# Performance work log

Measured on AMD Instinct MI355X. Metric: run time of the kernel, lower is better.

The kernel has to match this reference:

```python
import jax, jax.numpy as jnp
import numpy as np

EPS = 1e-5
B, C, H, W = 128, 512, 32, 32


def setup_inputs() -> dict:
    key = jax.random.key(0)
    ks = jax.random.split(key, 3)
    s = 1.0 / np.sqrt(C)
    return {
        "x": jax.random.normal(ks[0], (B, C, H, W), dtype=jnp.float32),
        "ln_w": jnp.ones((C, H, W), dtype=jnp.float32),
        "ln_b": jnp.zeros((C, H, W), dtype=jnp.float32),
        "w1": jax.random.uniform(ks[1], (C, C), dtype=jnp.float32, minval=-s, maxval=s),
        "b1": jnp.zeros((C,), dtype=jnp.float32),
        "w2": jax.random.uniform(ks[2], (C, C), dtype=jnp.float32, minval=-s, maxval=s),
        "b2": jnp.zeros((C,), dtype=jnp.float32),
    }


def reference(x, ln_w, ln_b, w1, b1, w2, b2):
    b, c, h, w = x.shape
    # LayerNorm over the full (C, H, W) feature volume per sample
    mu = jnp.mean(x, axis=(1, 2, 3), keepdims=True)
    var = jnp.mean(jnp.square(x - mu), axis=(1, 2, 3), keepdims=True)
    xn = (x - mu) * jax.lax.rsqrt(var + EPS) * ln_w + ln_b
    # tokens: (B, H*W, C)
    t = xn.reshape(b, c, h * w).transpose(0, 2, 1)
    hdn = jax.nn.relu(jnp.einsum('bsc,dc->bsd', t, w1) + b1)
    out = jnp.einsum('bsd,ed->bse', hdn, w2) + b2
    return out.transpose(0, 2, 1).reshape(b, c, h, w)
```

## Files before the change

### kernel.cpp

```cpp
#include <hip/hip_runtime.h>
#include <stdint.h>


#define NSAMP 128
#define CCH   512
#define HWSZ  1024
#define NPER  (CCH*HWSZ)

typedef unsigned short u16;
typedef __bf16 bf16x8 __attribute__((ext_vector_type(8)));
typedef float  f32x4  __attribute__((ext_vector_type(4)));

__device__ __forceinline__ float b2f(u16 h){ return __uint_as_float(((unsigned)h)<<16); }
__device__ __forceinline__ u16 f2b(float f){
  unsigned u = __float_as_uint(f);
  u += 0x7FFFu + ((u>>16)&1u);
  return (u16)(u>>16);
}
__device__ __forceinline__ void unpack8(uint4 v, float* f){
  const unsigned* u = (const unsigned*)&v;
#pragma unroll
  for (int q=0;q<4;q++){
    f[2*q]   = __uint_as_float(u[q]<<16);
    f[2*q+1] = __uint_as_float(u[q]&0xFFFF0000u);
  }
}
__device__ __forceinline__ void load8(const void* base, size_t idx, int isf, float* f){
  if (isf){
    const float* p = (const float*)base + idx;
    uint4 a = *(const uint4*)p;
    uint4 b = *(const uint4*)(p+4);
    const float* af = (const float*)&a;
    const float* bf = (const float*)&b;
#pragma unroll
    for (int j=0;j<4;j++){ f[j]=af[j]; f[4+j]=bf[j]; }
  } else {
    uint4 v = *(const uint4*)((const u16*)base + idx);
    unpack8(v, f);
  }
}
__device__ __forceinline__ void store8b(u16* dst, const float* f){
  uint4 o; unsigned* ou = (unsigned*)&o;
#pragma unroll
  for (int q=0;q<4;q++) ou[q] = (unsigned)f2b(f[2*q]) | ((unsigned)f2b(f[2*q+1])<<16);
  *(uint4*)dst = o;
}

__device__ __forceinline__ void gload_lds16(const u16* g, u16* l){
  __builtin_amdgcn_global_load_lds(
      (const __attribute__((address_space(1))) void*)g,
      (__attribute__((address_space(3))) void*)l,
      16, 0, 0);
}

__global__ __launch_bounds__(256) void detect_kernel(const u16* __restrict__ x,
                                                     int* __restrict__ flag){
  __shared__ int sh[256];
  int tid = threadIdx.x, cnt = 0;
  for (int i=tid; i<16384; i+=256){
    unsigned e = ((unsigned)x[i] >> 7) & 0xFFu;
    cnt += (e >= 0xC0u);
  }
  sh[tid] = cnt; __syncthreads();
  for (int s=128; s; s>>=1){ if (tid<s) sh[tid]+=sh[tid+s]; __syncthreads(); }
  if (tid==0) flag[0] = sh[0];
}

__global__ __launch_bounds__(256) void convert_kernel(
    const void* __restrict__ w1, const void* __restrict__ w2,
    const void* __restrict__ b1, const void* __restrict__ b2,
    const int* __restrict__ flag,
    u16* __restrict__ w1b, u16* __restrict__ w2b,
    float* __restrict__ b1f, float* __restrict__ b2f){
  int isf = flag[0] > 64;
  int t = blockIdx.x*256 + threadIdx.x;
  size_t i8 = (size_t)t*8;
  float f[8];
  load8(w1, i8, isf, f); store8b(w1b + i8, f);
  load8(w2, i8, isf, f); store8b(w2b + i8, f);
  if (t < 64){
    load8(b1, i8, isf, f);
#pragma unroll
    for (int j=0;j<8;j++) b1f[i8+j] = f[j];
    load8(b2, i8, isf, f);
#pragma unroll
    for (int j=0;j<8;j++) b2f[i8+j] = f[j];
  }
}

__global__ __launch_bounds__(256) void stats_kernel(const void* __restrict__ x,
                                                    float* __restrict__ stats,
                                                    const int* __restrict__ flag){
  int isf = flag[0] > 64;
  int b   = blockIdx.y;
  int blk = blockIdx.x;
  size_t base = (size_t)b*NPER + (size_t)blk*32768;
  int tid = threadIdx.x;
  float s1 = 0.f, s2 = 0.f;
#pragma unroll
  for (int i=0;i<16;i++){
    float f[8];
    load8(x, base + i*2048 + tid*8, isf, f);
#pragma unroll
    for (int j=0;j<8;j++){ s1 += f[j]; s2 += f[j]*f[j]; }
  }
#pragma unroll
  for (int off=32; off; off>>=1){
    s1 += __shfl_down(s1, off);
    s2 += __shfl_down(s2, off);
  }
  __shared__ float r1[4], r2[4];
  int w = tid>>6, lane = tid&63;
  if (lane==0){ r1[w]=s1; r2[w]=s2; }
  __syncthreads();
  if (tid==0){
    atomicAdd(&stats[2*b],   r1[0]+r1[1]+r1[2]+r1[3]);
    atomicAdd(&stats[2*b+1], r2[0]+r2[1]+r2[2]+r2[3]);
  }
}

__global__ __launch_bounds__(256) void lnT_kernel(const void* __restrict__ x,
                                                  const void* __restrict__ lw,
                                                  const void* __restrict__ lb,
                                                  const float* __restrict__ stats,
                                                  const int* __restrict__ flag,
                                                  int gb0,
                                                  u16* __restrict__ xnT){
  int isf = flag[0] > 64;
  int bl = blockIdx.z;
  int gb = gb0 + bl;
  int c0 = blockIdx.y*64;
  int s0 = blockIdx.x*64;
  const float invN = 1.f/(float)NPER;
  float mu  = stats[2*gb]*invN;
  float var = fmaxf(stats[2*gb+1]*invN - mu*mu, 0.f);
  float rs  = rsqrtf(var + 1e-5f);

  __shared__ float T[64][65];
  int tid = threadIdx.x;
  int tr  = tid>>3;
  int tcl = (tid&7)*8;

#pragma unroll
  for (int p=0;p<2;p++){
    int c = c0 + p*32 + tr;
    size_t idx = (size_t)c*HWSZ + s0 + tcl;
    float xf[8], wf[8], bf_[8];
    load8(x,  (size_t)gb*NPER + idx, isf, xf);
    load8(lw, idx, isf, wf);
    load8(lb, idx, isf, bf_);
    float* dst = &T[p*32 + tr][tcl];
#pragma unroll
    for (int j=0;j<8;j++) dst[j] = (xf[j]-mu)*rs*wf[j] + bf_[j];
  }
  __syncthreads();
#pragma unroll
  for (int p=0;p<2;p++){
    int srow = p*32 + tr;
    float tmp[8];
#pragma unroll
    for (int j=0;j<8;j++) tmp[j] = T[tcl+j][srow];
    store8b(xnT + ((size_t)bl*HWSZ + s0 + srow)*CCH + c0 + tcl, tmp);
  }
}

template<int RELU, int BIASM, int MFIRST, int NOUT, int DUALOUT>
__global__ __launch_bounds__(256) void gemm_kernel(
    const u16* __restrict__ A, long sA,
    const u16* __restrict__ B, long sB,
    const float* __restrict__ bias,
    u16* __restrict__ Co,
    const int* __restrict__ flag, int gb0)
{
  __shared__ __align__(16) u16 sh[32768];

  int b  = blockIdx.y;
  int bx = blockIdx.x;
  int tm, tn;
  if (MFIRST){ tm = bx & 7; tn = bx >> 3; }
  else       { tn = bx & 7; tm = bx >> 3; }
  const u16* Ab = A + (size_t)b*sA + (size_t)(tm*128)*512;
  const u16* Bb = B + (size_t)b*sB + (size_t)(tn*128)*512;

  int tid  = threadIdx.x;
  int lane = tid & 63;
  int w    = tid >> 6;
  int wm   = w >> 1, wn = w & 1;
  int l15  = lane & 15;
  int q    = lane >> 4;
  int sw   = l15 & 7;

  int ar  = tid >> 3;
  int acs = ((tid & 7) ^ (ar & 7)) * 8;
  const u16* aSrc = Ab + (size_t)ar*512 + acs;
  const u16* bSrc = Bb + (size_t)ar*512 + acs;

  f32x4 acc[4][4];
#pragma unroll
  for (int i=0;i<4;i++)
#pragma unroll
    for (int j=0;j<4;j++) acc[i][j] = (f32x4){0.f,0.f,0.f,0.f};

  auto STAGE = [&](int p, int kk){
    u16* aD = sh + p*16384 + tid*8;
    u16* bD = sh + p*16384 + 8192 + tid*8;
#pragma unroll
    for (int j=0;j<4;j++) gload_lds16(aSrc + j*16384 + kk, aD + j*2048);
#pragma unroll
    for (int j=0;j<4;j++) gload_lds16(bSrc + j*16384 + kk, bD + j*2048);
  };
  auto COMPUTE = [&](int p){
    const u16* Asb = sh + p*16384;
    const u16* Bsb = sh + p*16384 + 8192;
#pragma unroll
    for (int ks=0; ks<2; ks++){
      bf16x8 fa[4], fb[4];
      int pc = ((ks*4 + q) ^ sw) * 8;
#pragma unroll
      for (int i=0;i<4;i++){
        fa[i] = *(const bf16x8*)(Asb + (wm*64 + i*16 + l15)*64 + pc);
        fb[i] = *(const bf16x8*)(Bsb + (wn*64 + i*16 + l15)*64 + pc);
      }
#pragma unroll
      for (int i=0;i<4;i++)
#pragma unroll
        for (int jn=0;jn<4;jn++)
          acc[i][jn] = __builtin_amdgcn_mfma_f32_16x16x32_bf16(fa[i], fb[jn], acc[i][jn], 0,0,0);
    }
  };

  STAGE(0, 0);
  __syncthreads();
#pragma unroll
  for (int t=0; t<7; t++){
    int cur = t & 1;
    STAGE(cur ^ 1, (t+1)*64);
    COMPUTE(cur);
    __syncthreads();
  }
  COMPUTE(7 & 1);
  __syncthreads();

  int isf = DUALOUT ? (flag[0] > 64) : 0;
  size_t sampOff = (size_t)(gb0 + b) * NPER;
  int row0 = tm*128, col0 = tn*128;

  if (!DUALOUT || !isf){
    u16* Cb = Co + sampOff;
#pragma unroll
    for (int i=0;i<4;i++){
#pragma unroll
      for (int jn=0;jn<4;jn++){
        int n = wn*64 + jn*16 + l15;
        float bn = BIASM ? 0.f : bias[col0 + n];
#pragma unroll
        for (int r=0;r<4;r++){
          int m = wm*64 + i*16 + q*4 + r;
          float v = acc[i][jn][r] + (BIASM ? bias[row0 + m] : bn);
          if (RELU) v = fmaxf(v, 0.f);
          sh[m*128 + (n ^ ((m&7)<<3))] = f2b(v);
        }
      }
    }
    __syncthreads();
    int rr  = tid >> 1;
    int c0_ = (tid & 1)*8;
#pragma unroll
    for (int j=0;j<8;j++){
      int c = c0_ + j;
      uint4 vv = *(const uint4*)(sh + rr*128 + ((c ^ (rr&7))<<3));
      *(uint4*)(Cb + (size_t)(row0+rr)*NOUT + col0 + (c<<3)) = vv;
    }
  } else {
    float* Cf  = (float*)Co + sampOff;
    float* shf = (float*)sh;
#pragma unroll
    for (int p=0;p<2;p++){
      if (p) __syncthreads();
      if (wm == p){
#pragma unroll
        for (int i=0;i<4;i++){
#pragma unroll
          for (int jn=0;jn<4;jn++){
            int n = wn*64 + jn*16 + l15;
            float bn = BIASM ? 0.f : bias[col0 + n];
#pragma unroll
            for (int r=0;r<4;r++){
              int ml = i*16 + q*4 + r;
              float v = acc[i][jn][r] + (BIASM ? bias[row0 + p*64 + ml] : bn);
              if (RELU) v = fmaxf(v, 0.f);
              shf[ml*128 + (((n>>2) ^ (ml&7))<<2) + (n&3)] = v;
            }
          }
        }
      }
      __syncthreads();
      int rr = tid >> 2, qt = tid & 3;
#pragma unroll
      for (int j=0;j<8;j++){
        int c = qt*8 + j;
        uint4 vv = *(const uint4*)(shf + rr*128 + ((c ^ (rr&7))<<2));
        *(uint4*)(Cf + (size_t)(row0 + p*64 + rr)*NOUT + col0 + (c<<2)) = vv;
      }
    }
  }
}

extern "C" void kernel_launch(void* const* d_in, const int* in_sizes, int n_in,
                              void* d_out, int out_size, void* d_ws, size_t ws_size,
                              hipStream_t stream) {
  (void)in_sizes; (void)n_in; (void)out_size;
  const void* x  = d_in[0];
  const void* lw = d_in[1];
  const void* lb = d_in[2];
  const void* w1 = d_in[3];
  const void* b1 = d_in[4];
  const void* w2 = d_in[5];
  const void* b2 = d_in[6];

  char* ws = (char*)d_ws;
  float* stats = (float*)ws;
  int*   flag  = (int*)(ws + 1024);
  float* b1f   = (float*)(ws + 2048);
  float* b2f   = (float*)(ws + 4096);
  u16*   w1b   = (u16*)(ws + 8192);
  u16*   w2b   = (u16*)(ws + 8192 + 524288);
  u16*   xnT   = (u16*)(ws + (size_t)(2u<<20));

  long gmax = ((long)ws_size - (2L<<20)) / (2L<<20);
  int G = (int)(gmax < 1 ? 1 : (gmax > 128 ? 128 : gmax));
  u16* hdnT = xnT + (size_t)G*NPER;

  hipMemsetAsync(d_ws, 0, 2048, stream);
  detect_kernel<<<1,256,0,stream>>>((const u16*)x, flag);
  convert_kernel<<<128,256,0,stream>>>(w1, w2, b1, b2, flag, w1b, w2b, b1f, b2f);
  stats_kernel<<<dim3(16,NSAMP),256,0,stream>>>(x, stats, flag);

  for (int b0=0; b0<NSAMP; b0+=G){
    int Gi = (NSAMP-b0 < G) ? (NSAMP-b0) : G;
    lnT_kernel<<<dim3(HWSZ/64, CCH/64, Gi),256,0,stream>>>(x, lw, lb, stats, flag, b0, xnT);
    gemm_kernel<1,0,1,512,0><<<dim3(32,Gi),256,0,stream>>>(
        xnT, (long)NPER, w1b, 0L, b1f, hdnT, flag, 0);
    gemm_kernel<0,1,0,1024,1><<<dim3(32,Gi),256,0,stream>>>(
        w2b, 0L, hdnT, (long)NPER, b2f, (u16*)d_out, flag, b0);
  }
}
```

Measured before the change: 813.3 us.

## Pre-convert LN affine params to bf16, relax GEMM pipeline barriers, widen fp32 epilogue

```diff
diff --git a/kernel.cpp b/kernel.cpp
--- a/kernel.cpp
+++ b/kernel.cpp
@@ -69,15 +69,21 @@
 __global__ __launch_bounds__(256) void convert_kernel(
     const void* __restrict__ w1, const void* __restrict__ w2,
     const void* __restrict__ b1, const void* __restrict__ b2,
+    const void* __restrict__ lw, const void* __restrict__ lb,
     const int* __restrict__ flag,
     u16* __restrict__ w1b, u16* __restrict__ w2b,
-    float* __restrict__ b1f, float* __restrict__ b2f){
+    float* __restrict__ b1f, float* __restrict__ b2f,
+    u16* __restrict__ lwb, u16* __restrict__ lbb){
   int isf = flag[0] > 64;
   int t = blockIdx.x*256 + threadIdx.x;
   size_t i8 = (size_t)t*8;
   float f[8];
-  load8(w1, i8, isf, f); store8b(w1b + i8, f);
-  load8(w2, i8, isf, f); store8b(w2b + i8, f);
+  if (t < 32768){
+    load8(w1, i8, isf, f); store8b(w1b + i8, f);
+    load8(w2, i8, isf, f); store8b(w2b + i8, f);
+  }
+  load8(lw, i8, isf, f); store8b(lwb + i8, f);
+  load8(lb, i8, isf, f); store8b(lbb + i8, f);
   if (t < 64){
     load8(b1, i8, isf, f);
 #pragma unroll
@@ -120,8 +126,8 @@
 }
 
 __global__ __launch_bounds__(256) void lnT_kernel(const void* __restrict__ x,
-                                                  const void* __restrict__ lw,
-                                                  const void* __restrict__ lb,
+                                                  const u16* __restrict__ lwb,
+                                                  const u16* __restrict__ lbb,
                                                   const float* __restrict__ stats,
                                                   const int* __restrict__ flag,
                                                   int gb0,
@@ -146,9 +152,9 @@
     int c = c0 + p*32 + tr;
     size_t idx = (size_t)c*HWSZ + s0 + tcl;
     float xf[8], wf[8], bf_[8];
-    load8(x,  (size_t)gb*NPER + idx, isf, xf);
-    load8(lw, idx, isf, wf);
-    load8(lb, idx, isf, bf_);
+    load8(x, (size_t)gb*NPER + idx, isf, xf);
+    unpack8(*(const uint4*)(lwb + idx), wf);
+    unpack8(*(const uint4*)(lbb + idx), bf_);
     float* dst = &T[p*32 + tr][tcl];
 #pragma unroll
     for (int j=0;j<8;j++) dst[j] = (xf[j]-mu)*rs*wf[j] + bf_[j];
@@ -230,15 +236,19 @@
   };
 
   STAGE(0, 0);
-  __syncthreads();
 #pragma unroll
   for (int t=0; t<7; t++){
-    int cur = t & 1;
-    STAGE(cur ^ 1, (t+1)*64);
-    COMPUTE(cur);
-    __syncthreads();
-  }
-  COMPUTE(7 & 1);
+    STAGE((t+1)&1, (t+1)*64);
+    asm volatile("s_waitcnt vmcnt(8)" ::: "memory");
+    __builtin_amdgcn_s_barrier();
+    __builtin_amdgcn_sched_barrier(0);
+    COMPUTE(t & 1);
+    __builtin_amdgcn_s_barrier();
+  }
+  asm volatile("s_waitcnt vmcnt(0)" ::: "memory");
+  __builtin_amdgcn_s_barrier();
+  __builtin_amdgcn_sched_barrier(0);
+  COMPUTE(1);
   __syncthreads();
 
   int isf = DUALOUT ? (flag[0] > 64) : 0;
@@ -275,33 +285,28 @@
     float* Cf  = (float*)Co + sampOff;
     float* shf = (float*)sh;
 #pragma unroll
-    for (int p=0;p<2;p++){
-      if (p) __syncthreads();
-      if (wm == p){
-#pragma unroll
-        for (int i=0;i<4;i++){
-#pragma unroll
-          for (int jn=0;jn<4;jn++){
-            int n = wn*64 + jn*16 + l15;
-            float bn = BIASM ? 0.f : bias[col0 + n];
-#pragma unroll
-            for (int r=0;r<4;r++){
-              int ml = i*16 + q*4 + r;
-              float v = acc[i][jn][r] + (BIASM ? bias[row0 + p*64 + ml] : bn);
-              if (RELU) v = fmaxf(v, 0.f);
-              shf[ml*128 + (((n>>2) ^ (ml&7))<<2) + (n&3)] = v;
-            }
-          }
+    for (int i=0;i<4;i++){
+#pragma unroll
+      for (int jn=0;jn<4;jn++){
+        int n = wn*64 + jn*16 + l15;
+        float bn = BIASM ? 0.f : bias[col0 + n];
+#pragma unroll
+        for (int r=0;r<4;r++){
+          int m = wm*64 + i*16 + q*4 + r;
+          float v = acc[i][jn][r] + (BIASM ? bias[row0 + m] : bn);
+          if (RELU) v = fmaxf(v, 0.f);
+          shf[m*128 + (((n>>2) ^ (m&7))<<2) + (n&3)] = v;
         }
       }
-      __syncthreads();
-      int rr = tid >> 2, qt = tid & 3;
-#pragma unroll
-      for (int j=0;j<8;j++){
-        int c = qt*8 + j;
-        uint4 vv = *(const uint4*)(shf + rr*128 + ((c ^ (rr&7))<<2));
-        *(uint4*)(Cf + (size_t)(row0 + p*64 + rr)*NOUT + col0 + (c<<2)) = vv;
-      }
+    }
+    __syncthreads();
+    int rr = tid >> 1;
+    int hf = (tid & 1)*16;
+#pragma unroll
+    for (int j=0;j<16;j++){
+      int c = hf + j;
+      uint4 vv = *(const uint4*)(shf + rr*128 + ((c ^ (rr&7))<<2));
+      *(uint4*)(Cf + (size_t)(row0+rr)*NOUT + col0 + (c<<2)) = vv;
     }
   }
 }
@@ -325,20 +330,23 @@
   float* b2f   = (float*)(ws + 4096);
   u16*   w1b   = (u16*)(ws + 8192);
   u16*   w2b   = (u16*)(ws + 8192 + 524288);
-  u16*   xnT   = (u16*)(ws + (size_t)(2u<<20));
-
-  long gmax = ((long)ws_size - (2L<<20)) / (2L<<20);
+  u16*   lwb   = (u16*)(ws + 1179648);
+  u16*   lbb   = (u16*)(ws + 1179648 + 1048576);
+  u16*   xnT   = (u16*)(ws + (size_t)(4u<<20));
+
+  long gmax = ((long)ws_size - (4L<<20)) / (2L<<20);
   int G = (int)(gmax < 1 ? 1 : (gmax > 128 ? 128 : gmax));
   u16* hdnT = xnT + (size_t)G*NPER;
 
   hipMemsetAsync(d_ws, 0, 2048, stream);
   detect_kernel<<<1,256,0,stream>>>((const u16*)x, flag);
-  convert_kernel<<<128,256,0,stream>>>(w1, w2, b1, b2, flag, w1b, w2b, b1f, b2f);
+  convert_kernel<<<256,256,0,stream>>>(w1, w2, b1, b2, lw, lb, flag,
+                                       w1b, w2b, b1f, b2f, lwb, lbb);
   stats_kernel<<<dim3(16,NSAMP),256,0,stream>>>(x, stats, flag);
 
   for (int b0=0; b0<NSAMP; b0+=G){
     int Gi = (NSAMP-b0 < G) ? (NSAMP-b0) : G;
-    lnT_kernel<<<dim3(HWSZ/64, CCH/64, Gi),256,0,stream>>>(x, lw, lb, stats, flag, b0, xnT);
+    lnT_kernel<<<dim3(HWSZ/64, CCH/64, Gi),256,0,stream>>>(x, lwb, lbb, stats, flag, b0, xnT);
     gemm_kernel<1,0,1,512,0><<<dim3(32,Gi),256,0,stream>>>(
         xnT, (long)NPER, w1b, 0L, b1f, hdnT, flag, 0);
     gemm_kernel<0,1,0,1024,1><<<dim3(32,Gi),256,0,stream>>>(
```

Result: faster. 783.5 us (-3.7%).
